# Kernel tuning notes

Hardware: AMD Instinct MI355X
Metric: run time of the kernel (lower is better)

## Reference

```python
import jax, jax.numpy as jnp
import numpy as np

FEATURE_MAPS = [8, 4, 2, 1]
BOXES_PER_LOC = [4, 6, 6, 4]
IMAGE_SIZE = 128
DECODED_SIZE = 64
Z_WHAT = 64
CHANNELS = [64, 256, 128, 64, 32, 16, 3]  # conv-transpose pyramid 1x1 -> 64x64
BATCH = 4
EMPTY_CONST = -1000.0
N_LOC = sum(f * f for f in FEATURE_MAPS)            # 85
N_BOX = sum(f * f * b for f, b in zip(FEATURE_MAPS, BOXES_PER_LOC))  # 380


def _recon_indices():
    # Decoder.reconstruction_indices: expand per-location latents to per-box.
    idx, last = [], 0
    for fm, bpl in zip(FEATURE_MAPS, BOXES_PER_LOC):
        for i in range(fm * fm):
            idx.append(np.full(bpl, last + i, dtype=np.int32))
        last += fm * fm
    return np.concatenate(idx)


def setup_inputs() -> dict:
    key = jax.random.key(0)
    ks = jax.random.split(key, 16)
    inp = {
        'z_what': jax.random.normal(ks[0], (BATCH, N_LOC, Z_WHAT), jnp.float32),
        'z_where': jax.random.uniform(ks[1], (BATCH, N_BOX, 4), jnp.float32),
        'z_present': jax.random.randint(ks[2], (BATCH, N_BOX, 1), 0, 2).astype(jnp.int32),
        'z_depth': jax.random.normal(ks[3], (BATCH, N_LOC, 1), jnp.float32),
    }
    for i, (cin, cout) in enumerate(zip(CHANNELS[:-1], CHANNELS[1:])):
        inp[f'w{i}'] = jax.random.normal(ks[4 + i], (2, 2, cin, cout), jnp.float32) / np.sqrt(4.0 * cin)
        inp[f'b{i}'] = jnp.zeros((cout,), jnp.float32)
    return inp


def _what_decoder(z_flat, params):
    # (N, Z) -> (N, 3, 64, 64): stack of stride-2 kernel-2 conv transposes.
    x = z_flat[:, :, None, None]
    n = len(params)
    for i, (w, b) in enumerate(params):
        x = jax.lax.conv_transpose(x, w, strides=(2, 2), padding='VALID',
                                   dimension_numbers=('NCHW', 'HWIO', 'NCHW'))
        x = x + b[None, :, None, None]
        x = jax.nn.sigmoid(x) if i == n - 1 else jax.nn.relu(x)
    return x


def _sample_bilinear(img, px, py):
    # img (3, D, D); px/py (S,) pixel coords along cols/rows; zero outside.
    D = DECODED_SIZE
    x0 = jnp.floor(px)
    y0 = jnp.floor(py)
    wx = px - x0
    wy = py - y0

    def gather(yi, xi):
        vy = (yi >= 0) & (yi <= D - 1)
        vx = (xi >= 0) & (xi <= D - 1)
        yc = jnp.clip(yi.astype(jnp.int32), 0, D - 1)
        xc = jnp.clip(xi.astype(jnp.int32), 0, D - 1)
        vals = img[:, yc[:, None], xc[None, :]]  # (3, S, S)
        return vals * (vy[:, None] & vx[None, :]).astype(img.dtype)

    g00 = gather(y0, x0)
    g01 = gather(y0, x0 + 1)
    g10 = gather(y0 + 1, x0)
    g11 = gather(y0 + 1, x0 + 1)
    wyc = wy[None, :, None]
    wxc = wx[None, None, :]
    return (g00 * (1 - wyc) * (1 - wxc) + g01 * (1 - wyc) * wxc
            + g10 * wyc * (1 - wxc) + g11 * wyc * wxc)


def _where_stn(imgs, z_where):
    # Paste each decoded glyph into an IMAGE_SIZE canvas at box (cx, cy, w, h).
    S, D = IMAGE_SIZE, DECODED_SIZE
    cx, cy, w, h = (z_where[:, i] for i in range(4))
    sx = jnp.maximum(w, 1e-5)
    sy = jnp.maximum(h, 1e-5)
    out = jnp.linspace(-1.0, 1.0, S)
    xin = (out[None, :] - (2 * cx - 1)[:, None]) / sx[:, None]  # (N, S)
    yin = (out[None, :] - (2 * cy - 1)[:, None]) / sy[:, None]
    px = (xin + 1) * (D - 1) / 2
    py = (yin + 1) * (D - 1) / 2
    return jax.vmap(_sample_bilinear)(imgs, px, py)  # (N, 3, S, S)


def reference(z_what, z_where, z_present, z_depth, w0, b0, w1, b1, w2, b2, w3, b3, w4, b4, w5, b5):
    params = [(w0, b0), (w1, b1), (w2, b2), (w3, b3), (w4, b4), (w5, b5)]
    idx = jnp.asarray(_recon_indices())
    zw = jnp.take(z_what, idx, axis=1)   # (B, N_BOX, Z)
    zd = jnp.take(z_depth, idx, axis=1)  # (B, N_BOX, 1)
    B = zw.shape[0]
    decoded = _what_decoder(zw.reshape(B * N_BOX, Z_WHAT), params)
    transformed = _where_stn(decoded, z_where.reshape(B * N_BOX, 4))
    recon = transformed.reshape(B, N_BOX, 3, IMAGE_SIZE, IMAGE_SIZE)
    depths = jnp.where(z_present[..., 0] == 1, zd[..., 0], EMPTY_CONST)  # (B, N_BOX)
    weights = jax.nn.softmax(depths, axis=1)
    return jnp.einsum('bn,bnchw->bchw', weights, recon)
```

## Files before the change

kernel.cpp:

```cpp
#include <hip/hip_runtime.h>
#include <hip/hip_bf16.h>

#define NBOX  380
#define NLOCS 85
#define NINST 340
#define NSPLIT 8

__device__ __forceinline__ int loc_of_box(int n) {
    if (n < 256) return n >> 2;
    if (n < 352) return 64 + (n - 256) / 6;
    if (n < 376) return 80 + (n - 352) / 6;
    return 84;
}

__global__ void box_params_k(const float* __restrict__ zwhere,
                             const int* __restrict__ zpresent,
                             const float* __restrict__ zdepth,
                             float* __restrict__ wgt, float* __restrict__ sxs,
                             float* __restrict__ oxs, float* __restrict__ sys,
                             float* __restrict__ oys, int* __restrict__ binst,
                             int* __restrict__ rect, int* __restrict__ cidx,
                             int* __restrict__ cnt)
{
    int b = blockIdx.x;
    int tid = threadIdx.x;
    __shared__ float sd[NBOX];
    __shared__ float red[128];

    for (int n = tid; n < NBOX; n += 128) {
        int loc = loc_of_box(n);
        sd[n] = (zpresent[b * NBOX + n] == 1) ? zdepth[b * NLOCS + loc] : -1000.0f;
    }
    __syncthreads();

    float m = -1e30f;
    for (int n = tid; n < NBOX; n += 128) m = fmaxf(m, sd[n]);
    red[tid] = m; __syncthreads();
    for (int s = 64; s > 0; s >>= 1) {
        if (tid < s) red[tid] = fmaxf(red[tid], red[tid + s]);
        __syncthreads();
    }
    m = red[0]; __syncthreads();

    float sum = 0.0f;
    for (int n = tid; n < NBOX; n += 128) sum += expf(sd[n] - m);
    red[tid] = sum; __syncthreads();
    for (int s = 64; s > 0; s >>= 1) {
        if (tid < s) red[tid] += red[tid + s];
        __syncthreads();
    }
    float inv = 1.0f / red[0];
    __syncthreads();

    for (int n = tid; n < NBOX; n += 128) {
        int g = b * NBOX + n;
        float wv = expf(sd[n] - m) * inv;
        wgt[g] = wv;
        float cx = zwhere[g * 4 + 0], cy = zwhere[g * 4 + 1];
        float w  = zwhere[g * 4 + 2], h  = zwhere[g * 4 + 3];
        float isx = 1.0f / fmaxf(w, 1e-5f);
        float isy = 1.0f / fmaxf(h, 1e-5f);
        float sxv = isx * (63.0f / 127.0f);
        float oxv = 31.5f * (1.0f - 2.0f * cx * isx);
        float syv = isy * (63.0f / 127.0f);
        float oyv = 31.5f * (1.0f - 2.0f * cy * isy);
        sxs[g] = sxv; oxs[g] = oxv; sys[g] = syv; oys[g] = oyv;
        binst[g] = b * NLOCS + loc_of_box(n);
        int wlo = min(127, max(0, (int)floorf((-1.0f - oxv) / sxv)));
        int whi = max(0, min(127, (int)ceilf((64.0f - oxv) / sxv)));
        int hlo = min(127, max(0, (int)floorf((-1.0f - oyv) / syv)));
        int hhi = max(0, min(127, (int)ceilf((64.0f - oyv) / syv)));
        rect[g] = wlo | (whi << 8) | (hlo << 16) | (hhi << 24);
        sd[n] = wv;
    }
    __syncthreads();

    if (tid < 64) {
        int base = 0;
        for (int c = 0; c < 6; ++c) {
            int n = c * 64 + tid;
            bool p = (n < NBOX) && (sd[n] > 0.0f);
            unsigned long long mask = __ballot(p);
            int pos = __popcll(mask & ((1ull << tid) - 1ull));
            if (p) cidx[b * NBOX + base + pos] = n;
            base += __popcll(mask);
        }
        if (tid == 0) cnt[b] = base;
    }
}

__global__ __launch_bounds__(256) void decode_fused_k(
    const float* __restrict__ z_what,
    const float* __restrict__ W0, const float* __restrict__ B0,
    const float* __restrict__ W1, const float* __restrict__ B1,
    const float* __restrict__ W2, const float* __restrict__ B2,
    const float* __restrict__ W3, const float* __restrict__ B3,
    const float* __restrict__ W4, const float* __restrict__ B4,
    const float* __restrict__ W5, const float* __restrict__ B5,
    float* __restrict__ dec)
{
    __shared__ __align__(16) float sm[15552];
    float* s_x = sm;
    float* L0o = sm + 64;
    float* L1o = sm + 1088;
    float* L2o = sm + 3136;
    float* L4b = sm + 3136;
    float* L3o = sm + 7360;

    const int inst = blockIdx.x;
    const int tid = threadIdx.x;
    const int lane = tid & 63;
    const int wv = __builtin_amdgcn_readfirstlane(tid >> 6);

    if (tid < 64) s_x[tid] = z_what[inst * 64 + tid];
    __syncthreads();

    {
        float a0 = 0.f, a1 = 0.f, a2 = 0.f, a3 = 0.f;
        #pragma unroll 8
        for (int k = 0; k < 64; ++k) {
            float xv = s_x[k];
            a0 = fmaf(xv, W0[(3 * 64 + k) * 256 + tid], a0);
            a1 = fmaf(xv, W0[(2 * 64 + k) * 256 + tid], a1);
            a2 = fmaf(xv, W0[(1 * 64 + k) * 256 + tid], a2);
            a3 = fmaf(xv, W0[(0 * 64 + k) * 256 + tid], a3);
        }
        float bb = B0[tid];
        L0o[0 * 256 + tid] = fmaxf(a0 + bb, 0.f);
        L0o[1 * 256 + tid] = fmaxf(a1 + bb, 0.f);
        L0o[2 * 256 + tid] = fmaxf(a2 + bb, 0.f);
        L0o[3 * 256 + tid] = fmaxf(a3 + bb, 0.f);
    }
    __syncthreads();

    {
        const int co = tid & 127;
        const int th = __builtin_amdgcn_readfirstlane(tid >> 7);
        const int ftA = 3 - 2 * th;
        const int ftB = 2 - 2 * th;
        float accA[4] = {0.f, 0.f, 0.f, 0.f};
        float accB[4] = {0.f, 0.f, 0.f, 0.f};
        #pragma unroll 2
        for (int q = 0; q < 64; ++q) {
            int k0 = q * 4;
            float xr[4][4];
            *(float4*)xr[0] = *(const float4*)&L0o[0 * 256 + k0];
            *(float4*)xr[1] = *(const float4*)&L0o[1 * 256 + k0];
            *(float4*)xr[2] = *(const float4*)&L0o[2 * 256 + k0];
            *(float4*)xr[3] = *(const float4*)&L0o[3 * 256 + k0];
            #pragma unroll
            for (int kk = 0; kk < 4; ++kk) {
                int k = k0 + kk;
                float wA = W1[(ftA * 256 + k) * 128 + co];
                float wB = W1[(ftB * 256 + k) * 128 + co];
                #pragma unroll
                for (int p = 0; p < 4; ++p) {
                    accA[p] = fmaf(xr[p][kk], wA, accA[p]);
                    accB[p] = fmaf(xr[p][kk], wB, accB[p]);
                }
            }
        }
        float bb = B1[co];
        #pragma unroll
        for (int p = 0; p < 4; ++p) {
            int i = p >> 1, j = p & 1;
            int opb = (2 * i + th) * 4 + 2 * j;
            L1o[(opb + 0) * 128 + co] = fmaxf(accA[p] + bb, 0.f);
            L1o[(opb + 1) * 128 + co] = fmaxf(accB[p] + bb, 0.f);
        }
    }
    __syncthreads();

    {
        const int co = tid & 63;
        const int t = wv, ft = 3 - t, di = t >> 1, dj = t & 1;
        float acc[16];
        #pragma unroll
        for (int p = 0; p < 16; ++p) acc[p] = 0.f;
        #pragma unroll 2
        for (int q = 0; q < 32; ++q) {
            int k0 = q * 4;
            float wk[4];
            #pragma unroll
            for (int kk = 0; kk < 4; ++kk)
                wk[kk] = W2[(ft * 128 + k0 + kk) * 64 + co];
            #pragma unroll
            for (int p = 0; p < 16; ++p) {
                float4 xq = *(const float4*)&L1o[p * 128 + k0];
                acc[p] = fmaf(xq.x, wk[0], acc[p]);
                acc[p] = fmaf(xq.y, wk[1], acc[p]);
                acc[p] = fmaf(xq.z, wk[2], acc[p]);
                acc[p] = fmaf(xq.w, wk[3], acc[p]);
            }
        }
        float bb = B2[co];
        #pragma unroll
        for (int p = 0; p < 16; ++p) {
            int i = p >> 2, j = p & 3;
            int op = (2 * i + di) * 8 + 2 * j + dj;
            L2o[co * 66 + op] = fmaxf(acc[p] + bb, 0.f);
        }
    }
    __syncthreads();

    {
        const int di = wv >> 1, coh = wv & 1;
        const int ft0 = 3 - 2 * di, ft1 = 2 - 2 * di;
        float a0[16], a1[16];
        #pragma unroll
        for (int c = 0; c < 16; ++c) { a0[c] = 0.f; a1[c] = 0.f; }
        #pragma unroll 2
        for (int k = 0; k < 64; ++k) {
            float xv = L2o[k * 66 + lane];
            const float* w0p = W3 + (ft0 * 64 + k) * 32 + coh * 16;
            const float* w1p = W3 + (ft1 * 64 + k) * 32 + coh * 16;
            #pragma unroll
            for (int c = 0; c < 16; ++c) {
                a0[c] = fmaf(xv, w0p[c], a0[c]);
                a1[c] = fmaf(xv, w1p[c], a1[c]);
            }
        }
        int i = lane >> 3, j = lane & 7;
        #pragma unroll
        for (int c = 0; c < 16; ++c) {
            float bb = B3[coh * 16 + c];
            float2 v = make_float2(fmaxf(a0[c] + bb, 0.f), fmaxf(a1[c] + bb, 0.f));
            *(float2*)&L3o[(coh * 16 + c) * 256 + (2 * i + di) * 16 + 2 * j] = v;
        }
    }
    __syncthreads();

    const int t5 = wv, ft5 = 3 - t5, di5 = t5 >> 1, dj5 = t5 & 1;
    float w5r[16][3];
    #pragma unroll
    for (int k = 0; k < 16; ++k)
        #pragma unroll
        for (int c = 0; c < 3; ++c)
            w5r[k][c] = W5[(ft5 * 16 + k) * 3 + c];
    const float b50 = B5[0], b51 = B5[1], b52 = B5[2];

    for (int c4 = 0; c4 < 4; ++c4) {
        {
            const int di = wv >> 1, coh = wv & 1;
            const int ft0 = 3 - 2 * di, ft1 = 2 - 2 * di;
            float a0[8], a1[8];
            #pragma unroll
            for (int c = 0; c < 8; ++c) { a0[c] = 0.f; a1[c] = 0.f; }
            #pragma unroll 4
            for (int k = 0; k < 32; ++k) {
                float xv = L3o[k * 256 + 64 * c4 + lane];
                const float* w0p = W4 + (ft0 * 32 + k) * 16 + coh * 8;
                const float* w1p = W4 + (ft1 * 32 + k) * 16 + coh * 8;
                #pragma unroll
                for (int c = 0; c < 8; ++c) {
                    a0[c] = fmaf(xv, w0p[c], a0[c]);
                    a1[c] = fmaf(xv, w1p[c], a1[c]);
                }
            }
            int il = lane >> 4, j = lane & 15;
            #pragma unroll
            for (int c = 0; c < 8; ++c) {
                float bb = B4[coh * 8 + c];
                float2 v = make_float2(fmaxf(a0[c] + bb, 0.f), fmaxf(a1[c] + bb, 0.f));
                *(float2*)&L4b[(coh * 8 + c) * 258 + (2 * il + di) * 32 + 2 * j] = v;
            }
        }
        __syncthreads();
        {
            #pragma unroll
            for (int sub = 0; sub < 4; ++sub) {
                int pl = sub * 64 + lane;
                int r = pl >> 5, x5 = pl & 31;
                int y5 = 8 * c4 + r;
                float a0 = b50, a1 = b51, a2 = b52;
                #pragma unroll
                for (int k = 0; k < 16; ++k) {
                    float xv = L4b[k * 258 + pl];
                    a0 = fmaf(xv, w5r[k][0], a0);
                    a1 = fmaf(xv, w5r[k][1], a1);
                    a2 = fmaf(xv, w5r[k][2], a2);
                }
                a0 = 1.0f / (1.0f + expf(-a0));
                a1 = 1.0f / (1.0f + expf(-a1));
                a2 = 1.0f / (1.0f + expf(-a2));
                float* dp = dec + (size_t)inst * 12288
                          + (size_t)((2 * y5 + di5) * 64 + 2 * x5 + dj5) * 3;
                dp[0] = a0; dp[1] = a1; dp[2] = a2;
            }
        }
        __syncthreads();
    }
}

__global__ __launch_bounds__(256) void composite_k(
    const float* __restrict__ dec, const float* __restrict__ wgt,
    const float* __restrict__ sxs, const float* __restrict__ oxs,
    const float* __restrict__ sys, const float* __restrict__ oys,
    const int* __restrict__ binst, const int* __restrict__ rect,
    const int* __restrict__ cidx, const int* __restrict__ cnt,
    float* __restrict__ part)
{
    int b = blockIdx.z, s = blockIdx.y;
    int tx0 = (blockIdx.x & 7) << 4, ty0 = (blockIdx.x >> 3) << 4;
    int lx = threadIdx.x & 15, ly = threadIdx.x >> 4;
    int w = tx0 + lx, h = ty0 + ly;

    int nb = cnt[b];
    int lo = (nb * s) / NSPLIT, hi = (nb * (s + 1)) / NSPLIT;

    float fw = (float)w, fh = (float)h;
    float a0 = 0.f, a1 = 0.f, a2 = 0.f;
    for (int q = lo; q < hi; ++q) {
        int n = cidx[b * NBOX + q];
        int rc = rect[b * NBOX + n];
        int wlo = rc & 255, whi = (rc >> 8) & 255;
        int hlo = (rc >> 16) & 255, hhi = (rc >> 24) & 255;
        if (whi < tx0 || wlo > tx0 + 15 || hhi < ty0 || hlo > ty0 + 15) continue;
        int g = b * NBOX + n;
        float wg = wgt[g];
        float px = fmaf(fw, sxs[g], oxs[g]);
        float py = fmaf(fh, sys[g], oys[g]);
        float x0 = floorf(px), y0 = floorf(py);
        if (x0 < -1.0f || x0 > 63.0f || y0 < -1.0f || y0 > 63.0f) continue;
        float wx = px - x0, wy = py - y0;
        int ix = (int)x0, iy = (int)y0;
        int x0c = max(ix, 0), x1c = min(ix + 1, 63);
        int y0c = max(iy, 0), y1c = min(iy + 1, 63);
        float m00 = (ix >= 0 && iy >= 0) ? 1.f : 0.f;
        float m01 = (ix + 1 <= 63 && iy >= 0) ? 1.f : 0.f;
        float m10 = (ix >= 0 && iy + 1 <= 63) ? 1.f : 0.f;
        float m11 = (ix + 1 <= 63 && iy + 1 <= 63) ? 1.f : 0.f;
        float w00 = (1.f - wy) * (1.f - wx) * m00;
        float w01 = (1.f - wy) * wx * m01;
        float w10 = wy * (1.f - wx) * m10;
        float w11 = wy * wx * m11;
        const float* img = dec + (size_t)binst[g] * 12288;
        int b00 = (y0c * 64 + x0c) * 3, b01 = (y0c * 64 + x1c) * 3;
        int b10 = (y1c * 64 + x0c) * 3, b11 = (y1c * 64 + x1c) * 3;
        a0 += wg * (w00 * img[b00]   + w01 * img[b01]   + w10 * img[b10]   + w11 * img[b11]);
        a1 += wg * (w00 * img[b00+1] + w01 * img[b01+1] + w10 * img[b10+1] + w11 * img[b11+1]);
        a2 += wg * (w00 * img[b00+2] + w01 * img[b01+2] + w10 * img[b10+2] + w11 * img[b11+2]);
    }
    size_t pb = (size_t)(b * NSPLIT + s) * 49152 + (size_t)h * 128 + w;
    part[pb]         = a0;
    part[pb + 16384] = a1;
    part[pb + 32768] = a2;
}

__global__ void reduce_k(const float* __restrict__ part, float* __restrict__ out)
{
    int i = blockIdx.x * 256 + threadIdx.x;
    int b = i / 49152;
    int r = i - b * 49152;
    float v = 0.f;
    #pragma unroll
    for (int s = 0; s < NSPLIT; ++s) v += part[(size_t)(b * NSPLIT + s) * 49152 + r];
    out[i] = v;
}

extern "C" void kernel_launch(void* const* d_in, const int* in_sizes, int n_in,
                              void* d_out, int out_size, void* d_ws, size_t ws_size,
                              hipStream_t stream)
{
    const float* z_what    = (const float*)d_in[0];
    const float* z_where   = (const float*)d_in[1];
    const int*   z_present = (const int*)  d_in[2];
    const float* z_depth   = (const float*)d_in[3];

    char* ws = (char*)d_ws;
    float* dec  = (float*)ws;
    float* part = (float*)(ws + 16711680);
    float* P    = (float*)(ws + 23003136);
    float* wgt = P,        *sxs = P + 1520, *oxs = P + 2 * 1520;
    float* sys = P + 3 * 1520, *oys = P + 4 * 1520;
    int* binst = (int*)(P + 5 * 1520);
    int* rect  = binst + 1520;
    int* cidx  = binst + 2 * 1520;
    int* cnt   = binst + 3 * 1520;

    box_params_k<<<dim3(4), dim3(128), 0, stream>>>(z_where, z_present, z_depth,
        wgt, sxs, oxs, sys, oys, binst, rect, cidx, cnt);

    decode_fused_k<<<dim3(NINST), dim3(256), 0, stream>>>(
        z_what,
        (const float*)d_in[4],  (const float*)d_in[5],
        (const float*)d_in[6],  (const float*)d_in[7],
        (const float*)d_in[8],  (const float*)d_in[9],
        (const float*)d_in[10], (const float*)d_in[11],
        (const float*)d_in[12], (const float*)d_in[13],
        (const float*)d_in[14], (const float*)d_in[15],
        dec);

    composite_k<<<dim3(64, NSPLIT, 4), dim3(256), 0, stream>>>(
        dec, wgt, sxs, oxs, sys, oys, binst, rect, cidx, cnt, part);
    reduce_k<<<dim3(768), dim3(256), 0, stream>>>(part, (float*)d_out);
}
```

Baseline: 99.32 us.

## Fuse box-params into decoder, widen decoder blocks, reduce splits in-block

Box-parameter computation now runs as four extra blocks of the decoder launch, which removes one kernel launch. The decoder moves from 256 to 512 threads per block, with each layer's work repartitioned across twice as many waves and a smaller shared-memory footprint. The composite kernel uses 1024-thread blocks holding four box splits and sums them through shared memory, replacing the global partial buffer and the separate reduce kernel. In exchange, there are fewer blocks per CU, split parallelism drops from 8 to 4, and register pressure may rise under the 512-thread launch bound.

```diff
diff --git a/kernel.cpp b/kernel.cpp
--- a/kernel.cpp
+++ b/kernel.cpp
@@ -4,7 +4,6 @@
 #define NBOX  380
 #define NLOCS 85
 #define NINST 340
-#define NSPLIT 8
 
 __device__ __forceinline__ int loc_of_box(int n) {
     if (n < 256) return n >> 2;
@@ -13,48 +12,41 @@
     return 84;
 }
 
-__global__ void box_params_k(const float* __restrict__ zwhere,
-                             const int* __restrict__ zpresent,
-                             const float* __restrict__ zdepth,
-                             float* __restrict__ wgt, float* __restrict__ sxs,
-                             float* __restrict__ oxs, float* __restrict__ sys,
-                             float* __restrict__ oys, int* __restrict__ binst,
-                             int* __restrict__ rect, int* __restrict__ cidx,
-                             int* __restrict__ cnt)
+__device__ void box_params_dev(int b, const float* __restrict__ zwhere,
+    const int* __restrict__ zpresent, const float* __restrict__ zdepth,
+    float* wgt, float* sxs, float* oxs, float* sys, float* oys,
+    int* binst, int* rect, int* cidx, int* cnt, float* sm)
 {
-    int b = blockIdx.x;
-    int tid = threadIdx.x;
-    __shared__ float sd[NBOX];
-    __shared__ float red[128];
-
-    for (int n = tid; n < NBOX; n += 128) {
-        int loc = loc_of_box(n);
-        sd[n] = (zpresent[b * NBOX + n] == 1) ? zdepth[b * NLOCS + loc] : -1000.0f;
-    }
-    __syncthreads();
-
-    float m = -1e30f;
-    for (int n = tid; n < NBOX; n += 128) m = fmaxf(m, sd[n]);
+    float* sd  = sm;
+    float* red = sm + 384;
+    const int tid = threadIdx.x;
+
+    if (tid < NBOX) {
+        int loc = loc_of_box(tid);
+        sd[tid] = (zpresent[b * NBOX + tid] == 1) ? zdepth[b * NLOCS + loc] : -1000.0f;
+    }
+    __syncthreads();
+
+    float m = (tid < NBOX) ? sd[tid] : -1e30f;
     red[tid] = m; __syncthreads();
-    for (int s = 64; s > 0; s >>= 1) {
+    for (int s = 256; s > 0; s >>= 1) {
         if (tid < s) red[tid] = fmaxf(red[tid], red[tid + s]);
         __syncthreads();
     }
     m = red[0]; __syncthreads();
 
-    float sum = 0.0f;
-    for (int n = tid; n < NBOX; n += 128) sum += expf(sd[n] - m);
+    float sum = (tid < NBOX) ? expf(sd[tid] - m) : 0.f;
     red[tid] = sum; __syncthreads();
-    for (int s = 64; s > 0; s >>= 1) {
+    for (int s = 256; s > 0; s >>= 1) {
         if (tid < s) red[tid] += red[tid + s];
         __syncthreads();
     }
     float inv = 1.0f / red[0];
     __syncthreads();
 
-    for (int n = tid; n < NBOX; n += 128) {
-        int g = b * NBOX + n;
-        float wv = expf(sd[n] - m) * inv;
+    if (tid < NBOX) {
+        int g = b * NBOX + tid;
+        float wv = expf(sd[tid] - m) * inv;
         wgt[g] = wv;
         float cx = zwhere[g * 4 + 0], cy = zwhere[g * 4 + 1];
         float w  = zwhere[g * 4 + 2], h  = zwhere[g * 4 + 3];
@@ -65,13 +57,13 @@
         float syv = isy * (63.0f / 127.0f);
         float oyv = 31.5f * (1.0f - 2.0f * cy * isy);
         sxs[g] = sxv; oxs[g] = oxv; sys[g] = syv; oys[g] = oyv;
-        binst[g] = b * NLOCS + loc_of_box(n);
+        binst[g] = b * NLOCS + loc_of_box(tid);
         int wlo = min(127, max(0, (int)floorf((-1.0f - oxv) / sxv)));
         int whi = max(0, min(127, (int)ceilf((64.0f - oxv) / sxv)));
         int hlo = min(127, max(0, (int)floorf((-1.0f - oyv) / syv)));
         int hhi = max(0, min(127, (int)ceilf((64.0f - oyv) / syv)));
         rect[g] = wlo | (whi << 8) | (hlo << 16) | (hhi << 24);
-        sd[n] = wv;
+        sd[tid] = wv;
     }
     __syncthreads();
 
@@ -89,7 +81,7 @@
     }
 }
 
-__global__ __launch_bounds__(256) void decode_fused_k(
+__global__ __launch_bounds__(512, 4) void decode_fused_k(
     const float* __restrict__ z_what,
     const float* __restrict__ W0, const float* __restrict__ B0,
     const float* __restrict__ W1, const float* __restrict__ B1,
@@ -97,15 +89,27 @@
     const float* __restrict__ W3, const float* __restrict__ B3,
     const float* __restrict__ W4, const float* __restrict__ B4,
     const float* __restrict__ W5, const float* __restrict__ B5,
+    const float* __restrict__ z_where, const int* __restrict__ z_present,
+    const float* __restrict__ z_depth,
+    float* __restrict__ wgt, float* __restrict__ sxs, float* __restrict__ oxs,
+    float* __restrict__ sys, float* __restrict__ oys, int* __restrict__ binst,
+    int* __restrict__ rect, int* __restrict__ cidx, int* __restrict__ cnt,
     float* __restrict__ dec)
 {
-    __shared__ __align__(16) float sm[15552];
-    float* s_x = sm;
-    float* L0o = sm + 64;
-    float* L1o = sm + 1088;
-    float* L2o = sm + 3136;
-    float* L4b = sm + 3136;
-    float* L3o = sm + 7360;
+    __shared__ __align__(16) float sm[12416];
+
+    if (blockIdx.x >= NINST) {
+        box_params_dev(blockIdx.x - NINST, z_where, z_present, z_depth,
+                       wgt, sxs, oxs, sys, oys, binst, rect, cidx, cnt, sm);
+        return;
+    }
+
+    float* L2o = sm;
+    float* s_x = sm + 4224;
+    float* L0o = sm + 4288;
+    float* L1o = sm + 5312;
+    float* L3o = sm + 4224;
+    float* L4b = sm;
 
     const int inst = blockIdx.x;
     const int tid = threadIdx.x;
@@ -116,121 +120,118 @@
     __syncthreads();
 
     {
-        float a0 = 0.f, a1 = 0.f, a2 = 0.f, a3 = 0.f;
+        const int co = tid & 255;
+        const int tg = __builtin_amdgcn_readfirstlane(tid >> 8);
+        const float* wA = W0 + (size_t)(3 - tg) * 64 * 256 + co;
+        const float* wB = W0 + (size_t)(1 - tg) * 64 * 256 + co;
+        float a0 = 0.f, a1 = 0.f;
         #pragma unroll 8
         for (int k = 0; k < 64; ++k) {
             float xv = s_x[k];
-            a0 = fmaf(xv, W0[(3 * 64 + k) * 256 + tid], a0);
-            a1 = fmaf(xv, W0[(2 * 64 + k) * 256 + tid], a1);
-            a2 = fmaf(xv, W0[(1 * 64 + k) * 256 + tid], a2);
-            a3 = fmaf(xv, W0[(0 * 64 + k) * 256 + tid], a3);
-        }
-        float bb = B0[tid];
-        L0o[0 * 256 + tid] = fmaxf(a0 + bb, 0.f);
-        L0o[1 * 256 + tid] = fmaxf(a1 + bb, 0.f);
-        L0o[2 * 256 + tid] = fmaxf(a2 + bb, 0.f);
-        L0o[3 * 256 + tid] = fmaxf(a3 + bb, 0.f);
+            a0 = fmaf(xv, wA[k * 256], a0);
+            a1 = fmaf(xv, wB[k * 256], a1);
+        }
+        float bb = B0[co];
+        L0o[tg * 256 + co]       = fmaxf(a0 + bb, 0.f);
+        L0o[(tg + 2) * 256 + co] = fmaxf(a1 + bb, 0.f);
     }
     __syncthreads();
 
     {
         const int co = tid & 127;
-        const int th = __builtin_amdgcn_readfirstlane(tid >> 7);
-        const int ftA = 3 - 2 * th;
-        const int ftB = 2 - 2 * th;
-        float accA[4] = {0.f, 0.f, 0.f, 0.f};
-        float accB[4] = {0.f, 0.f, 0.f, 0.f};
+        const int t = __builtin_amdgcn_readfirstlane(tid >> 7);
+        const int ft = 3 - t, di = t >> 1, dj = t & 1;
+        const float* wp = W1 + (size_t)ft * 256 * 128 + co;
+        float acc[4] = {0.f, 0.f, 0.f, 0.f};
         #pragma unroll 2
         for (int q = 0; q < 64; ++q) {
             int k0 = q * 4;
-            float xr[4][4];
-            *(float4*)xr[0] = *(const float4*)&L0o[0 * 256 + k0];
-            *(float4*)xr[1] = *(const float4*)&L0o[1 * 256 + k0];
-            *(float4*)xr[2] = *(const float4*)&L0o[2 * 256 + k0];
-            *(float4*)xr[3] = *(const float4*)&L0o[3 * 256 + k0];
-            #pragma unroll
-            for (int kk = 0; kk < 4; ++kk) {
-                int k = k0 + kk;
-                float wA = W1[(ftA * 256 + k) * 128 + co];
-                float wB = W1[(ftB * 256 + k) * 128 + co];
-                #pragma unroll
-                for (int p = 0; p < 4; ++p) {
-                    accA[p] = fmaf(xr[p][kk], wA, accA[p]);
-                    accB[p] = fmaf(xr[p][kk], wB, accB[p]);
-                }
-            }
+            float4 x0 = *(const float4*)&L0o[0 * 256 + k0];
+            float4 x1 = *(const float4*)&L0o[1 * 256 + k0];
+            float4 x2 = *(const float4*)&L0o[2 * 256 + k0];
+            float4 x3 = *(const float4*)&L0o[3 * 256 + k0];
+            float w0 = wp[(k0 + 0) * 128], w1 = wp[(k0 + 1) * 128];
+            float w2 = wp[(k0 + 2) * 128], w3 = wp[(k0 + 3) * 128];
+            acc[0] = fmaf(x0.x, w0, acc[0]); acc[0] = fmaf(x0.y, w1, acc[0]);
+            acc[0] = fmaf(x0.z, w2, acc[0]); acc[0] = fmaf(x0.w, w3, acc[0]);
+            acc[1] = fmaf(x1.x, w0, acc[1]); acc[1] = fmaf(x1.y, w1, acc[1]);
+            acc[1] = fmaf(x1.z, w2, acc[1]); acc[1] = fmaf(x1.w, w3, acc[1]);
+            acc[2] = fmaf(x2.x, w0, acc[2]); acc[2] = fmaf(x2.y, w1, acc[2]);
+            acc[2] = fmaf(x2.z, w2, acc[2]); acc[2] = fmaf(x2.w, w3, acc[2]);
+            acc[3] = fmaf(x3.x, w0, acc[3]); acc[3] = fmaf(x3.y, w1, acc[3]);
+            acc[3] = fmaf(x3.z, w2, acc[3]); acc[3] = fmaf(x3.w, w3, acc[3]);
         }
         float bb = B1[co];
         #pragma unroll
         for (int p = 0; p < 4; ++p) {
             int i = p >> 1, j = p & 1;
-            int opb = (2 * i + th) * 4 + 2 * j;
-            L1o[(opb + 0) * 128 + co] = fmaxf(accA[p] + bb, 0.f);
-            L1o[(opb + 1) * 128 + co] = fmaxf(accB[p] + bb, 0.f);
+            L1o[((2 * i + di) * 4 + 2 * j + dj) * 128 + co] = fmaxf(acc[p] + bb, 0.f);
         }
     }
     __syncthreads();
 
     {
-        const int co = tid & 63;
-        const int t = wv, ft = 3 - t, di = t >> 1, dj = t & 1;
-        float acc[16];
-        #pragma unroll
-        for (int p = 0; p < 16; ++p) acc[p] = 0.f;
+        const int co = lane;
+        const int t = wv & 3, ih = wv >> 2;
+        const int ft = 3 - t, di = t >> 1, dj = t & 1;
+        const float* wp = W2 + (size_t)ft * 128 * 64 + co;
+        float acc[8] = {0.f,0.f,0.f,0.f,0.f,0.f,0.f,0.f};
         #pragma unroll 2
         for (int q = 0; q < 32; ++q) {
             int k0 = q * 4;
-            float wk[4];
-            #pragma unroll
-            for (int kk = 0; kk < 4; ++kk)
-                wk[kk] = W2[(ft * 128 + k0 + kk) * 64 + co];
-            #pragma unroll
-            for (int p = 0; p < 16; ++p) {
-                float4 xq = *(const float4*)&L1o[p * 128 + k0];
-                acc[p] = fmaf(xq.x, wk[0], acc[p]);
-                acc[p] = fmaf(xq.y, wk[1], acc[p]);
-                acc[p] = fmaf(xq.z, wk[2], acc[p]);
-                acc[p] = fmaf(xq.w, wk[3], acc[p]);
+            float w0 = wp[(k0 + 0) * 64], w1 = wp[(k0 + 1) * 64];
+            float w2 = wp[(k0 + 2) * 64], w3 = wp[(k0 + 3) * 64];
+            #pragma unroll
+            for (int pp = 0; pp < 8; ++pp) {
+                float4 xq = *(const float4*)&L1o[(ih * 8 + pp) * 128 + k0];
+                acc[pp] = fmaf(xq.x, w0, acc[pp]);
+                acc[pp] = fmaf(xq.y, w1, acc[pp]);
+                acc[pp] = fmaf(xq.z, w2, acc[pp]);
+                acc[pp] = fmaf(xq.w, w3, acc[pp]);
             }
         }
         float bb = B2[co];
         #pragma unroll
-        for (int p = 0; p < 16; ++p) {
+        for (int pp = 0; pp < 8; ++pp) {
+            int p = ih * 8 + pp;
             int i = p >> 2, j = p & 3;
             int op = (2 * i + di) * 8 + 2 * j + dj;
-            L2o[co * 66 + op] = fmaxf(acc[p] + bb, 0.f);
+            L2o[co * 66 + op] = fmaxf(acc[pp] + bb, 0.f);
         }
     }
     __syncthreads();
 
     {
-        const int di = wv >> 1, coh = wv & 1;
+        const int di = wv >> 2, coq = wv & 3;
         const int ft0 = 3 - 2 * di, ft1 = 2 - 2 * di;
-        float a0[16], a1[16];
-        #pragma unroll
-        for (int c = 0; c < 16; ++c) { a0[c] = 0.f; a1[c] = 0.f; }
-        #pragma unroll 2
+        const float* w0b = W3 + (size_t)ft0 * 64 * 32 + coq * 8;
+        const float* w1b = W3 + (size_t)ft1 * 64 * 32 + coq * 8;
+        float a0[8], a1[8];
+        #pragma unroll
+        for (int c = 0; c < 8; ++c) { a0[c] = 0.f; a1[c] = 0.f; }
+        #pragma unroll 4
         for (int k = 0; k < 64; ++k) {
             float xv = L2o[k * 66 + lane];
-            const float* w0p = W3 + (ft0 * 64 + k) * 32 + coh * 16;
-            const float* w1p = W3 + (ft1 * 64 + k) * 32 + coh * 16;
-            #pragma unroll
-            for (int c = 0; c < 16; ++c) {
+            const float* w0p = w0b + k * 32;
+            const float* w1p = w1b + k * 32;
+            #pragma unroll
+            for (int c = 0; c < 8; ++c) {
                 a0[c] = fmaf(xv, w0p[c], a0[c]);
                 a1[c] = fmaf(xv, w1p[c], a1[c]);
             }
         }
         int i = lane >> 3, j = lane & 7;
         #pragma unroll
-        for (int c = 0; c < 16; ++c) {
-            float bb = B3[coh * 16 + c];
+        for (int c = 0; c < 8; ++c) {
+            float bb = B3[coq * 8 + c];
             float2 v = make_float2(fmaxf(a0[c] + bb, 0.f), fmaxf(a1[c] + bb, 0.f));
-            *(float2*)&L3o[(coh * 16 + c) * 256 + (2 * i + di) * 16 + 2 * j] = v;
-        }
-    }
-    __syncthreads();
-
-    const int t5 = wv, ft5 = 3 - t5, di5 = t5 >> 1, dj5 = t5 & 1;
+            *(float2*)&L3o[(coq * 8 + c) * 256 + (2 * i + di) * 16 + 2 * j] = v;
+        }
+    }
+    __syncthreads();
+
+    const int t5 = wv & 3, pxh5 = wv >> 2;
+    const int ft5 = 3 - t5, di5 = t5 >> 1, dj5 = t5 & 1;
     float w5r[16][3];
     #pragma unroll
     for (int k = 0; k < 16; ++k)
@@ -241,39 +242,41 @@
 
     for (int c4 = 0; c4 < 4; ++c4) {
         {
-            const int di = wv >> 1, coh = wv & 1;
-            const int ft0 = 3 - 2 * di, ft1 = 2 - 2 * di;
-            float a0[8], a1[8];
-            #pragma unroll
-            for (int c = 0; c < 8; ++c) { a0[c] = 0.f; a1[c] = 0.f; }
+            const int di4 = wv >> 2, coq4 = wv & 3;
+            const int ft0 = 3 - 2 * di4, ft1 = 2 - 2 * di4;
+            const float* w0b = W4 + (size_t)ft0 * 32 * 16 + coq4 * 4;
+            const float* w1b = W4 + (size_t)ft1 * 32 * 16 + coq4 * 4;
+            float a0[4], a1[4];
+            #pragma unroll
+            for (int c = 0; c < 4; ++c) { a0[c] = 0.f; a1[c] = 0.f; }
             #pragma unroll 4
             for (int k = 0; k < 32; ++k) {
                 float xv = L3o[k * 256 + 64 * c4 + lane];
-                const float* w0p = W4 + (ft0 * 32 + k) * 16 + coh * 8;
-                const float* w1p = W4 + (ft1 * 32 + k) * 16 + coh * 8;
+                const float* w0p = w0b + k * 16;
+                const float* w1p = w1b + k * 16;
                 #pragma unroll
-                for (int c = 0; c < 8; ++c) {
+                for (int c = 0; c < 4; ++c) {
                     a0[c] = fmaf(xv, w0p[c], a0[c]);
                     a1[c] = fmaf(xv, w1p[c], a1[c]);
                 }
             }
             int il = lane >> 4, j = lane & 15;
             #pragma unroll
-            for (int c = 0; c < 8; ++c) {
-                float bb = B4[coh * 8 + c];
+            for (int c = 0; c < 4; ++c) {
+                float bb = B4[coq4 * 4 + c];
                 float2 v = make_float2(fmaxf(a0[c] + bb, 0.f), fmaxf(a1[c] + bb, 0.f));
-                *(float2*)&L4b[(coh * 8 + c) * 258 + (2 * il + di) * 32 + 2 * j] = v;
+                *(float2*)&L4b[(coq4 * 4 + c) * 258 + (2 * il + di4) * 32 + 2 * j] = v;
             }
         }
         __syncthreads();
         {
             #pragma unroll
-            for (int sub = 0; sub < 4; ++sub) {
-                int pl = sub * 64 + lane;
+            for (int sub = 0; sub < 2; ++sub) {
+                int pl = pxh5 * 128 + sub * 64 + lane;
                 int r = pl >> 5, x5 = pl & 31;
                 int y5 = 8 * c4 + r;
                 float a0 = b50, a1 = b51, a2 = b52;
-                #pragma unroll
+                #pragma unroll 4
                 for (int k = 0; k < 16; ++k) {
                     float xv = L4b[k * 258 + pl];
                     a0 = fmaf(xv, w5r[k][0], a0);
@@ -292,21 +295,24 @@
     }
 }
 
-__global__ __launch_bounds__(256) void composite_k(
+__global__ __launch_bounds__(1024) void composite_k(
     const float* __restrict__ dec, const float* __restrict__ wgt,
     const float* __restrict__ sxs, const float* __restrict__ oxs,
     const float* __restrict__ sys, const float* __restrict__ oys,
     const int* __restrict__ binst, const int* __restrict__ rect,
     const int* __restrict__ cidx, const int* __restrict__ cnt,
-    float* __restrict__ part)
+    float* __restrict__ out)
 {
-    int b = blockIdx.z, s = blockIdx.y;
-    int tx0 = (blockIdx.x & 7) << 4, ty0 = (blockIdx.x >> 3) << 4;
-    int lx = threadIdx.x & 15, ly = threadIdx.x >> 4;
+    __shared__ float pls[4][256][3];
+
+    int b = blockIdx.x >> 6, tile = blockIdx.x & 63;
+    int tx0 = (tile & 7) << 4, ty0 = (tile >> 3) << 4;
+    int s = threadIdx.x >> 8, px = threadIdx.x & 255;
+    int lx = px & 15, ly = px >> 4;
     int w = tx0 + lx, h = ty0 + ly;
 
     int nb = cnt[b];
-    int lo = (nb * s) / NSPLIT, hi = (nb * (s + 1)) / NSPLIT;
+    int lo = (nb * s) >> 2, hi = (nb * (s + 1)) >> 2;
 
     float fw = (float)w, fh = (float)h;
     float a0 = 0.f, a1 = 0.f, a2 = 0.f;
@@ -318,11 +324,11 @@
         if (whi < tx0 || wlo > tx0 + 15 || hhi < ty0 || hlo > ty0 + 15) continue;
         int g = b * NBOX + n;
         float wg = wgt[g];
-        float px = fmaf(fw, sxs[g], oxs[g]);
-        float py = fmaf(fh, sys[g], oys[g]);
-        float x0 = floorf(px), y0 = floorf(py);
+        float pxx = fmaf(fw, sxs[g], oxs[g]);
+        float pyy = fmaf(fh, sys[g], oys[g]);
+        float x0 = floorf(pxx), y0 = floorf(pyy);
         if (x0 < -1.0f || x0 > 63.0f || y0 < -1.0f || y0 > 63.0f) continue;
-        float wx = px - x0, wy = py - y0;
+        float wx = pxx - x0, wy = pyy - y0;
         int ix = (int)x0, iy = (int)y0;
         int x0c = max(ix, 0), x1c = min(ix + 1, 63);
         int y0c = max(iy, 0), y1c = min(iy + 1, 63);
@@ -341,21 +347,15 @@
         a1 += wg * (w00 * img[b00+1] + w01 * img[b01+1] + w10 * img[b10+1] + w11 * img[b11+1]);
         a2 += wg * (w00 * img[b00+2] + w01 * img[b01+2] + w10 * img[b10+2] + w11 * img[b11+2]);
     }
-    size_t pb = (size_t)(b * NSPLIT + s) * 49152 + (size_t)h * 128 + w;
-    part[pb]         = a0;
-    part[pb + 16384] = a1;
-    part[pb + 32768] = a2;
-}
-
-__global__ void reduce_k(const float* __restrict__ part, float* __restrict__ out)
-{
-    int i = blockIdx.x * 256 + threadIdx.x;
-    int b = i / 49152;
-    int r = i - b * 49152;
-    float v = 0.f;
-    #pragma unroll
-    for (int s = 0; s < NSPLIT; ++s) v += part[(size_t)(b * NSPLIT + s) * 49152 + r];
-    out[i] = v;
+    pls[s][px][0] = a0; pls[s][px][1] = a1; pls[s][px][2] = a2;
+    __syncthreads();
+
+    if (threadIdx.x < 768) {
+        int c = threadIdx.x >> 8, p2 = threadIdx.x & 255;
+        float v = pls[0][p2][c] + pls[1][p2][c] + pls[2][p2][c] + pls[3][p2][c];
+        int h2 = ty0 + (p2 >> 4), w2 = tx0 + (p2 & 15);
+        out[((b * 3 + c) * 128 + h2) * 128 + w2] = v;
+    }
 }
 
 extern "C" void kernel_launch(void* const* d_in, const int* in_sizes, int n_in,
@@ -368,9 +368,8 @@
     const float* z_depth   = (const float*)d_in[3];
 
     char* ws = (char*)d_ws;
-    float* dec  = (float*)ws;
-    float* part = (float*)(ws + 16711680);
-    float* P    = (float*)(ws + 23003136);
+    float* dec = (float*)ws;
+    float* P   = (float*)(ws + 16711680);
     float* wgt = P,        *sxs = P + 1520, *oxs = P + 2 * 1520;
     float* sys = P + 3 * 1520, *oys = P + 4 * 1520;
     int* binst = (int*)(P + 5 * 1520);
@@ -378,10 +377,7 @@
     int* cidx  = binst + 2 * 1520;
     int* cnt   = binst + 3 * 1520;
 
-    box_params_k<<<dim3(4), dim3(128), 0, stream>>>(z_where, z_present, z_depth,
-        wgt, sxs, oxs, sys, oys, binst, rect, cidx, cnt);
-
-    decode_fused_k<<<dim3(NINST), dim3(256), 0, stream>>>(
+    decode_fused_k<<<dim3(NINST + 4), dim3(512), 0, stream>>>(
         z_what,
         (const float*)d_in[4],  (const float*)d_in[5],
         (const float*)d_in[6],  (const float*)d_in[7],
@@ -389,9 +385,10 @@
         (const float*)d_in[10], (const float*)d_in[11],
         (const float*)d_in[12], (const float*)d_in[13],
         (const float*)d_in[14], (const float*)d_in[15],
+        z_where, z_present, z_depth,
+        wgt, sxs, oxs, sys, oys, binst, rect, cidx, cnt,
         dec);
 
-    composite_k<<<dim3(64, NSPLIT, 4), dim3(256), 0, stream>>>(
-        dec, wgt, sxs, oxs, sys, oys, binst, rect, cidx, cnt, part);
-    reduce_k<<<dim3(768), dim3(256), 0, stream>>>(part, (float*)d_out);
-}
+    composite_k<<<dim3(256), dim3(1024), 0, stream>>>(
+        dec, wgt, sxs, oxs, sys, oys, binst, rect, cidx, cnt, (float*)d_out);
+}
```

Result: slower. 136.6 us (+37.6%).
